# Kernel optimization log

Measured on AMD Instinct MI355X. Metric: run time of the kernel, lower is better.

Reference implementation:

```python
import jax, jax.numpy as jnp
import numpy as np
from jax import lax


def _conv(x, w, b, padding):
    # x: NCHW, w: OIHW
    y = lax.conv_general_dilated(x, w, (1, 1), padding,
                                 dimension_numbers=('NCHW', 'OIHW', 'NCHW'))
    return y + b[None, :, None, None]


def setup_inputs() -> dict:
    key = jax.random.key(0)
    ks = jax.random.split(key, 24)
    B = 64
    d = {
        'p2': jax.random.normal(ks[0], (B, 128, 64, 128), jnp.float32),
        'p3': jax.random.normal(ks[1], (B, 128, 32, 64), jnp.float32),
        'p4': jax.random.normal(ks[2], (B, 128, 16, 32), jnp.float32),
        'p5': jax.random.normal(ks[3], (B, 512, 8, 16), jnp.float32),
    }
    def w(k, shape, fan_in):
        return jax.random.normal(k, shape, jnp.float32) * (1.0 / np.sqrt(fan_in))
    # smooth convs 3x3, 128->128
    for i, name in enumerate(['s1', 's2', 's3']):
        d['w_' + name] = w(ks[4 + 2 * i], (128, 128, 3, 3), 128 * 9)
        d['b_' + name] = jnp.zeros((128,), jnp.float32)
    # tidy convs 1x1
    tidy_cin = [128, 128, 128, 512]
    for i in range(4):
        d['w_t%d' % (i + 1)] = w(ks[10 + i], (1, tidy_cin[i], 1, 1), tidy_cin[i])
        d['b_t%d' % (i + 1)] = jnp.zeros((1,), jnp.float32)
    # pl convs (kH,1) on single channel
    pl_kh = [64, 32, 16, 8]
    for i in range(4):
        d['w_pl%d' % (i + 1)] = w(ks[14 + i], (1, 1, pl_kh[i], 1), pl_kh[i])
        d['b_pl%d' % (i + 1)] = jnp.zeros((1,), jnp.float32)
    return d


def reference(p2, p3, p4, p5,
              w_s1, b_s1, w_s2, b_s2, w_s3, b_s3,
              w_t1, b_t1, w_t2, b_t2, w_t3, b_t3, w_t4, b_t4,
              w_pl1, b_pl1, w_pl2, b_pl2, w_pl3, b_pl3, w_pl4, b_pl4):
    B = p2.shape[0]
    # smooth + relu (p5 has no smooth in the original module)
    q2 = jax.nn.relu(_conv(p2, w_s1, b_s1, 'SAME'))
    q3 = jax.nn.relu(_conv(p3, w_s2, b_s2, 'SAME'))
    q4 = jax.nn.relu(_conv(p4, w_s3, b_s3, 'SAME'))
    # tidy 1x1 -> single score channel
    t1 = _conv(q2, w_t1, b_t1, 'VALID')
    t2 = _conv(q3, w_t2, b_t2, 'VALID')
    t3 = _conv(q4, w_t3, b_t3, 'VALID')
    t4 = _conv(p5, w_t4, b_t4, 'VALID')
    # column-pooling convs collapse height to 1 -> per-column scores
    c1 = _conv(t1, w_pl1, b_pl1, 'VALID').reshape(B, -1)  # [B,128]
    c2 = _conv(t2, w_pl2, b_pl2, 'VALID').reshape(B, -1)  # [B,64]
    c3 = _conv(t3, w_pl3, b_pl3, 'VALID').reshape(B, -1)  # [B,32]
    c4 = _conv(t4, w_pl4, b_pl4, 'VALID').reshape(B, -1)  # [B,16]
    return jnp.concatenate([c1, c2, c3, c4], axis=1)      # [B,240]
```

## Files before the change

### kernel.cpp

```cpp
#include <hip/hip_runtime.h>


typedef short s8v __attribute__((ext_vector_type(8)));
typedef float f4v __attribute__((ext_vector_type(4)));

#define BARRIER() asm volatile("s_waitcnt lgkmcnt(0)\n\ts_barrier" ::: "memory")

__device__ __forceinline__ unsigned short f32_bf16_rne(float f) {
  union { float f; unsigned int u; } v;
  v.f = f;
  unsigned int u = v.u;
  u += 0x7FFFu + ((u >> 16) & 1u);
  return (unsigned short)(u >> 16);
}

__global__ void prep_w_k(const float* __restrict__ w1,
                         const float* __restrict__ w2,
                         const float* __restrict__ w3,
                         unsigned short* __restrict__ out) {
  int idx = blockIdx.x * 256 + threadIdx.x;
  if (idx >= 442368) return;
  int i    = idx & 7;
  int cout = (idx >> 3) & 127;
  int t    = idx >> 10;
  int qg = t & 3; t >>= 2;
  int kw = t % 3; t /= 3;
  int kh = t % 3; t /= 3;
  int chunk = t & 3; t >>= 2;
  int s = t;
  const float* w = (s == 0) ? w1 : ((s == 1) ? w2 : w3);
  int cin = chunk * 32 + qg * 8 + i;
  out[idx] = f32_bf16_rne(w[((cout * 128 + cin) * 3 + kh) * 3 + kw]);
}

__global__ void init_out_k(float* __restrict__ out,
                           const float* bt1, const float* bt2,
                           const float* bt3, const float* bt4,
                           const float* wpl1, const float* bpl1,
                           const float* wpl2, const float* bpl2,
                           const float* wpl3, const float* bpl3,
                           const float* wpl4, const float* bpl4) {
  int idx = blockIdx.x * 256 + threadIdx.x;
  if (idx >= 64 * 240) return;
  int c = idx % 240;
  const float* wpl; const float* bpl; const float* bt; int H;
  if (c < 128)      { wpl = wpl1; bpl = bpl1; bt = bt1; H = 64; }
  else if (c < 192) { wpl = wpl2; bpl = bpl2; bt = bt2; H = 32; }
  else if (c < 224) { wpl = wpl3; bpl = bpl3; bt = bt3; H = 16; }
  else              { wpl = wpl4; bpl = bpl4; bt = bt4; H = 8;  }
  float s = 0.f;
  for (int h = 0; h < H; ++h) s += wpl[h];
  out[idx] = bt[0] * s + bpl[0];
}

__global__ void level4_k(const float* __restrict__ p5,
                         const float* __restrict__ w_t4,
                         const float* __restrict__ w_pl4,
                         float* __restrict__ out) {
  int b = blockIdx.x;
  int z = blockIdx.y;
  int t = threadIdx.x;
  int w = t & 15, g = t >> 4;
  const float* base = p5 + (size_t)b * 65536 + z * 16384;
  const float* wt = w_t4 + z * 128;
  float acc = 0.f;
  for (int j = g; j < 1024; j += 16) {
    acc += wt[j >> 3] * w_pl4[j & 7] * base[j * 16 + w];
  }
  acc += __shfl_xor(acc, 16);
  acc += __shfl_xor(acc, 32);
  if ((t & 48) == 0) atomicAdd(&out[b * 240 + 224 + w], acc);
}

template<int H, int W, int COLBASE>
__global__ __launch_bounds__(512, 1)
void conv_fused_k(const float* __restrict__ p,
                  const unsigned short* __restrict__ wl,
                  const float* __restrict__ b_s,
                  const float* __restrict__ w_t,
                  const float* __restrict__ w_pl,
                  float* __restrict__ out) {
  constexpr int R  = 4;
  constexpr int WP = W + 2;
  constexpr int HW = H * W;
  constexpr int WN = W / 16;
  constexpr int WM = 8 / WN;
  constexpr int MT = 8 / WM;
  constexpr int SLOTS = 2 * 4 * W;
  constexpr int SPT = (SLOTS + 511) / 512;

  __shared__ __align__(16) unsigned short Xs[2][4][6][WP][8];
  __shared__ __align__(16) unsigned short Ws[2][3][4][128][8];

  const int tid  = threadIdx.x;
  const int wave = tid >> 6, lane = tid & 63;
  const int lm = lane & 15, q = lane >> 4;
  const int mw = wave / WN, ns = wave % WN;
  const int hb = blockIdx.x * R;
  const int b  = blockIdx.y;
  const float* pb = p + (size_t)b * 128 * HW;

  bool sok[SPT];
  int  h0k[SPT];
  int  xbase[SPT];
  const float* sbase[SPT];
#pragma unroll
  for (int k = 0; k < SPT; ++k) {
    int slot = tid + 512 * k;
    sok[k] = (SLOTS % 512 == 0) ? true : (slot < SLOTS);
    int rk = slot / (4 * W);
    int qg = (slot / W) & 3;
    int wp = slot % W;
    h0k[k]   = hb - 1 + rk;
    xbase[k] = ((qg * 6 + rk) * WP + 1 + wp) * 8;
    sbase[k] = pb + (size_t)(qg * 8) * HW + wp;
  }

  float xf[SPT][8];
  s8v wreg[3];
  const unsigned short* wseg = wl + tid * 24;
  unsigned short* wdst = &Ws[0][0][0][0][0] + tid * 24;

  auto issueW = [&](int t) {
    const unsigned short* s = wseg + t * 12288;
#pragma unroll
    for (int j = 0; j < 3; ++j) wreg[j] = *(const s8v*)(s + j * 8);
  };
  auto writeW = [&](int buf) {
    unsigned short* d = wdst + buf * 12288;
#pragma unroll
    for (int j = 0; j < 3; ++j) *(s8v*)(d + j * 8) = wreg[j];
  };
  auto issueXa = [&](float (*arr)[8], int chunk, int kh) {
#pragma unroll
    for (int k = 0; k < SPT; ++k) {
      int hin = h0k[k] + 2 * kh;
      bool ok = sok[k] && ((unsigned)hin < (unsigned)H);
      if (ok) {
        const float* s = sbase[k] + (size_t)chunk * (32 * HW) + (size_t)hin * W;
#pragma unroll
        for (int i = 0; i < 8; ++i) arr[k][i] = s[(size_t)i * HW];
      } else {
#pragma unroll
        for (int i = 0; i < 8; ++i) arr[k][i] = 0.f;
      }
    }
  };
  auto writeXa = [&](float (*arr)[8], int buf, int kh) {
    unsigned short* dst = &Xs[buf][0][0][0][0] + 2 * kh * (WP * 8);
#pragma unroll
    for (int k = 0; k < SPT; ++k) {
      if (sok[k]) {
        s8v v;
#pragma unroll
        for (int i = 0; i < 8; ++i) v[i] = (short)f32_bf16_rne(arr[k][i]);
        *(s8v*)(dst + xbase[k]) = v;
      }
    }
  };

  if (tid < 96) {
    int t = tid;
    int pos = (t & 1) ? (WP - 1) : 0; t >>= 1;
    int sl = t % 6; t /= 6;
    int qg = t & 3; int bf = t >> 2;
    const s8v Z = {0, 0, 0, 0, 0, 0, 0, 0};
    *(s8v*)&Xs[bf][qg][sl][pos][0] = Z;
  }
  {
    float x0[SPT][8], x1[SPT][8], x2[SPT][8];
    issueW(0);
    issueXa(x0, 0, 0);
    issueXa(x1, 0, 1);
    issueXa(x2, 0, 2);
    writeW(0);
    issueW(1);
    writeXa(x0, 0, 0);
    writeXa(x1, 0, 1);
    writeXa(x2, 0, 2);
    issueXa(xf, 1, 0);
  }
  BARRIER();

  f4v acc[R][MT];
#pragma unroll
  for (int r = 0; r < R; ++r)
#pragma unroll
    for (int mt = 0; mt < MT; ++mt)
      acc[r][mt] = (f4v){0.f, 0.f, 0.f, 0.f};

  const int ncol = ns * 16 + lm;

  for (int c = 0; c < 4; ++c) {
#pragma unroll
    for (int kh = 0; kh < 3; ++kh) {
      const int sidx = c * 3 + kh;
      if (sidx < 11) writeW((sidx + 1) & 1);
      if (sidx < 10) issueW(sidx + 2);
      if (c < 3) writeXa(xf, (c + 1) & 1, kh);
      if (kh < 2) { if (c < 3) issueXa(xf, c + 1, kh + 1); }
      else        { if (c < 2) issueXa(xf, c + 2, 0); }

      const unsigned short* WsRd = &Ws[sidx & 1][0][0][0][0];
      const unsigned short* XsRd = &Xs[c & 1][0][0][0][0];
      __builtin_amdgcn_s_setprio(1);
#pragma unroll
      for (int kw = 0; kw < 3; ++kw) {
        s8v af[MT];
#pragma unroll
        for (int mt = 0; mt < MT; ++mt)
          af[mt] = *(const s8v*)(WsRd + kw * 4096 + q * 1024 +
                                 ((mw * MT + mt) * 16 + lm) * 8);
#pragma unroll
        for (int r = 0; r < R; ++r) {
          const s8v bfv = *(const s8v*)(XsRd + ((q * 6 + (kh + r)) * WP + (ncol + kw)) * 8);
#pragma unroll
          for (int mt = 0; mt < MT; ++mt)
            acc[r][mt] = __builtin_amdgcn_mfma_f32_16x16x32_bf16(af[mt], bfv, acc[r][mt], 0, 0, 0);
        }
      }
      __builtin_amdgcn_s_setprio(0);
      if (sidx < 11) BARRIER();
    }
  }

  float stot = 0.f;
#pragma unroll
  for (int r = 0; r < R; ++r) {
    float s = 0.f;
#pragma unroll
    for (int mt = 0; mt < MT; ++mt) {
#pragma unroll
      for (int rg = 0; rg < 4; ++rg) {
        int cout = (mw * MT + mt) * 16 + q * 4 + rg;
        float v = fmaxf(acc[r][mt][rg] + b_s[cout], 0.f);
        s = fmaf(w_t[cout], v, s);
      }
    }
    stot = fmaf(w_pl[hb + r], s, stot);
  }
  stot += __shfl_xor(stot, 16);
  stot += __shfl_xor(stot, 32);
  if (lane < 16) atomicAdd(&out[b * 240 + COLBASE + ncol], stot);
}

extern "C" void kernel_launch(void* const* d_in, const int* in_sizes, int n_in,
                              void* d_out, int out_size, void* d_ws, size_t ws_size,
                              hipStream_t stream) {
  (void)in_sizes; (void)n_in; (void)out_size; (void)ws_size;
  const float* p2   = (const float*)d_in[0];
  const float* p3   = (const float*)d_in[1];
  const float* p4   = (const float*)d_in[2];
  const float* p5   = (const float*)d_in[3];
  const float* w_s1 = (const float*)d_in[4];
  const float* b_s1 = (const float*)d_in[5];
  const float* w_s2 = (const float*)d_in[6];
  const float* b_s2 = (const float*)d_in[7];
  const float* w_s3 = (const float*)d_in[8];
  const float* b_s3 = (const float*)d_in[9];
  const float* w_t1 = (const float*)d_in[10];
  const float* b_t1 = (const float*)d_in[11];
  const float* w_t2 = (const float*)d_in[12];
  const float* b_t2 = (const float*)d_in[13];
  const float* w_t3 = (const float*)d_in[14];
  const float* b_t3 = (const float*)d_in[15];
  const float* w_t4 = (const float*)d_in[16];
  const float* b_t4 = (const float*)d_in[17];
  const float* w_pl1 = (const float*)d_in[18];
  const float* b_pl1 = (const float*)d_in[19];
  const float* w_pl2 = (const float*)d_in[20];
  const float* b_pl2 = (const float*)d_in[21];
  const float* w_pl3 = (const float*)d_in[22];
  const float* b_pl3 = (const float*)d_in[23];
  const float* w_pl4 = (const float*)d_in[24];
  const float* b_pl4 = (const float*)d_in[25];

  unsigned short* wp = (unsigned short*)d_ws;
  float* out = (float*)d_out;

  prep_w_k<<<dim3(1728), dim3(256), 0, stream>>>(w_s1, w_s2, w_s3, wp);
  init_out_k<<<dim3(60), dim3(256), 0, stream>>>(out, b_t1, b_t2, b_t3, b_t4,
                                                 w_pl1, b_pl1, w_pl2, b_pl2,
                                                 w_pl3, b_pl3, w_pl4, b_pl4);
  conv_fused_k<64, 128, 0><<<dim3(16, 64), dim3(512), 0, stream>>>(
      p2, wp, b_s1, w_t1, w_pl1, out);
  conv_fused_k<32, 64, 128><<<dim3(8, 64), dim3(512), 0, stream>>>(
      p3, wp + 147456, b_s2, w_t2, w_pl2, out);
  conv_fused_k<16, 32, 192><<<dim3(4, 64), dim3(512), 0, stream>>>(
      p4, wp + 294912, b_s3, w_t3, w_pl3, out);
  level4_k<<<dim3(64, 4), dim3(256), 0, stream>>>(p5, w_t4, w_pl4, out);
}
```

Baseline: 727.4 us.

## Shrink conv blocks to 256 threads with per-level row tiles and multi-column waves

The fused 3x3 conv kernels now run with 256 threads (4 waves) per block instead of 512. The largest level switches to 2 output rows per block, which doubles the grid. Each wave now covers several 16-column N tiles, so each B fragment is reused across more accumulators. The staging buffer, halo zeroing, weight-copy pattern and epilogue are generalised to the variable row count. The aim is better occupancy and load balance with smaller per-block LDS, traded against more halo re-reads for level 1 and more per-thread load work.

```diff
diff --git a/kernel.cpp b/kernel.cpp
--- a/kernel.cpp
+++ b/kernel.cpp
@@ -73,23 +73,25 @@
 }
 
 template<int H, int W, int COLBASE>
-__global__ __launch_bounds__(512, 1)
+__global__ __launch_bounds__(256, 1)
 void conv_fused_k(const float* __restrict__ p,
                   const unsigned short* __restrict__ wl,
                   const float* __restrict__ b_s,
                   const float* __restrict__ w_t,
                   const float* __restrict__ w_pl,
                   float* __restrict__ out) {
-  constexpr int R  = 4;
+  constexpr int R  = (W == 128) ? 2 : 4;
+  constexpr int RS = R + 2;
+  constexpr int NB = RS / 2;
   constexpr int WP = W + 2;
   constexpr int HW = H * W;
-  constexpr int WN = W / 16;
-  constexpr int WM = 8 / WN;
+  constexpr int WN = (W >= 64) ? 4 : 2;
+  constexpr int WM = 4 / WN;
+  constexpr int NT = (W / 16) / WN;
   constexpr int MT = 8 / WM;
-  constexpr int SLOTS = 2 * 4 * W;
-  constexpr int SPT = (SLOTS + 511) / 512;
-
-  __shared__ __align__(16) unsigned short Xs[2][4][6][WP][8];
+  constexpr int SPT = (2 * 4 * W) / 256;
+
+  __shared__ __align__(16) unsigned short Xs[2][4][RS][WP][8];
   __shared__ __align__(16) unsigned short Ws[2][3][4][128][8];
 
   const int tid  = threadIdx.x;
@@ -100,43 +102,38 @@
   const int b  = blockIdx.y;
   const float* pb = p + (size_t)b * 128 * HW;
 
-  bool sok[SPT];
-  int  h0k[SPT];
-  int  xbase[SPT];
-  const float* sbase[SPT];
+  int rk0[SPT]; int xb[SPT]; const float* sbase[SPT];
 #pragma unroll
   for (int k = 0; k < SPT; ++k) {
-    int slot = tid + 512 * k;
-    sok[k] = (SLOTS % 512 == 0) ? true : (slot < SLOTS);
+    int slot = tid + 256 * k;
     int rk = slot / (4 * W);
     int qg = (slot / W) & 3;
     int wp = slot % W;
-    h0k[k]   = hb - 1 + rk;
-    xbase[k] = ((qg * 6 + rk) * WP + 1 + wp) * 8;
+    rk0[k] = rk;
+    xb[k]  = ((qg * RS + rk) * WP + 1 + wp) * 8;
     sbase[k] = pb + (size_t)(qg * 8) * HW + wp;
   }
 
   float xf[SPT][8];
-  s8v wreg[3];
-  const unsigned short* wseg = wl + tid * 24;
-  unsigned short* wdst = &Ws[0][0][0][0][0] + tid * 24;
+  s8v wreg[6];
+  const unsigned short* wseg = wl + wave * 512 + lane * 8;
+  unsigned short* wdst = &Ws[0][0][0][0][0] + wave * 512 + lane * 8;
 
   auto issueW = [&](int t) {
     const unsigned short* s = wseg + t * 12288;
 #pragma unroll
-    for (int j = 0; j < 3; ++j) wreg[j] = *(const s8v*)(s + j * 8);
+    for (int j = 0; j < 6; ++j) wreg[j] = *(const s8v*)(s + j * 2048);
   };
   auto writeW = [&](int buf) {
     unsigned short* d = wdst + buf * 12288;
 #pragma unroll
-    for (int j = 0; j < 3; ++j) *(s8v*)(d + j * 8) = wreg[j];
-  };
-  auto issueXa = [&](float (*arr)[8], int chunk, int kh) {
+    for (int j = 0; j < 6; ++j) *(s8v*)(d + j * 2048) = wreg[j];
+  };
+  auto issueXa = [&](float (*arr)[8], int chunk, int burst) {
 #pragma unroll
     for (int k = 0; k < SPT; ++k) {
-      int hin = h0k[k] + 2 * kh;
-      bool ok = sok[k] && ((unsigned)hin < (unsigned)H);
-      if (ok) {
+      int hin = hb - 1 + 2 * burst + rk0[k];
+      if ((unsigned)hin < (unsigned)H) {
         const float* s = sbase[k] + (size_t)chunk * (32 * HW) + (size_t)hin * W;
 #pragma unroll
         for (int i = 0; i < 8; ++i) arr[k][i] = s[(size_t)i * HW];
@@ -146,50 +143,47 @@
       }
     }
   };
-  auto writeXa = [&](float (*arr)[8], int buf, int kh) {
-    unsigned short* dst = &Xs[buf][0][0][0][0] + 2 * kh * (WP * 8);
+  auto writeXa = [&](float (*arr)[8], int buf, int burst) {
+    unsigned short* dst = &Xs[buf][0][0][0][0] + 2 * burst * (WP * 8);
 #pragma unroll
     for (int k = 0; k < SPT; ++k) {
-      if (sok[k]) {
-        s8v v;
-#pragma unroll
-        for (int i = 0; i < 8; ++i) v[i] = (short)f32_bf16_rne(arr[k][i]);
-        *(s8v*)(dst + xbase[k]) = v;
-      }
-    }
-  };
-
-  if (tid < 96) {
-    int t = tid;
-    int pos = (t & 1) ? (WP - 1) : 0; t >>= 1;
-    int sl = t % 6; t /= 6;
-    int qg = t & 3; int bf = t >> 2;
+      s8v v;
+#pragma unroll
+      for (int i = 0; i < 8; ++i) v[i] = (short)f32_bf16_rne(arr[k][i]);
+      *(s8v*)(dst + xb[k]) = v;
+    }
+  };
+
+  if (tid < 16 * RS) {
+    int idx = tid;
+    int bf  = idx / (8 * RS); int rem = idx % (8 * RS);
+    int qg  = rem / (2 * RS); int r2  = rem % (2 * RS);
+    int sl  = r2 >> 1;
+    int pos = (r2 & 1) ? (WP - 1) : 0;
     const s8v Z = {0, 0, 0, 0, 0, 0, 0, 0};
     *(s8v*)&Xs[bf][qg][sl][pos][0] = Z;
   }
   {
-    float x0[SPT][8], x1[SPT][8], x2[SPT][8];
+    float xp[NB][SPT][8];
     issueW(0);
-    issueXa(x0, 0, 0);
-    issueXa(x1, 0, 1);
-    issueXa(x2, 0, 2);
+#pragma unroll
+    for (int j = 0; j < NB; ++j) issueXa(xp[j], 0, j);
     writeW(0);
     issueW(1);
-    writeXa(x0, 0, 0);
-    writeXa(x1, 0, 1);
-    writeXa(x2, 0, 2);
+#pragma unroll
+    for (int j = 0; j < NB; ++j) writeXa(xp[j], 0, j);
     issueXa(xf, 1, 0);
   }
   BARRIER();
 
-  f4v acc[R][MT];
+  f4v acc[R][MT][NT];
 #pragma unroll
   for (int r = 0; r < R; ++r)
 #pragma unroll
     for (int mt = 0; mt < MT; ++mt)
-      acc[r][mt] = (f4v){0.f, 0.f, 0.f, 0.f};
-
-  const int ncol = ns * 16 + lm;
+#pragma unroll
+      for (int t = 0; t < NT; ++t)
+        acc[r][mt][t] = (f4v){0.f, 0.f, 0.f, 0.f};
 
   for (int c = 0; c < 4; ++c) {
 #pragma unroll
@@ -197,9 +191,9 @@
       const int sidx = c * 3 + kh;
       if (sidx < 11) writeW((sidx + 1) & 1);
       if (sidx < 10) issueW(sidx + 2);
-      if (c < 3) writeXa(xf, (c + 1) & 1, kh);
-      if (kh < 2) { if (c < 3) issueXa(xf, c + 1, kh + 1); }
-      else        { if (c < 2) issueXa(xf, c + 2, 0); }
+      if (kh < NB) { if (c < 3) writeXa(xf, (c + 1) & 1, kh); }
+      if (kh + 1 < NB) { if (c < 3) issueXa(xf, c + 1, kh + 1); }
+      else if (kh == 2) { if (c < 2) issueXa(xf, c + 2, 0); }
 
       const unsigned short* WsRd = &Ws[sidx & 1][0][0][0][0];
       const unsigned short* XsRd = &Xs[c & 1][0][0][0][0];
@@ -212,36 +206,42 @@
           af[mt] = *(const s8v*)(WsRd + kw * 4096 + q * 1024 +
                                  ((mw * MT + mt) * 16 + lm) * 8);
 #pragma unroll
-        for (int r = 0; r < R; ++r) {
-          const s8v bfv = *(const s8v*)(XsRd + ((q * 6 + (kh + r)) * WP + (ncol + kw)) * 8);
-#pragma unroll
-          for (int mt = 0; mt < MT; ++mt)
-            acc[r][mt] = __builtin_amdgcn_mfma_f32_16x16x32_bf16(af[mt], bfv, acc[r][mt], 0, 0, 0);
-        }
+        for (int r = 0; r < R; ++r)
+#pragma unroll
+          for (int t = 0; t < NT; ++t) {
+            const int n = (ns * NT + t) * 16 + lm;
+            const s8v bfv = *(const s8v*)(XsRd + ((q * RS + (kh + r)) * WP + (n + kw)) * 8);
+#pragma unroll
+            for (int mt = 0; mt < MT; ++mt)
+              acc[r][mt][t] = __builtin_amdgcn_mfma_f32_16x16x32_bf16(af[mt], bfv, acc[r][mt][t], 0, 0, 0);
+          }
       }
       __builtin_amdgcn_s_setprio(0);
       if (sidx < 11) BARRIER();
     }
   }
 
-  float stot = 0.f;
-#pragma unroll
-  for (int r = 0; r < R; ++r) {
-    float s = 0.f;
-#pragma unroll
-    for (int mt = 0; mt < MT; ++mt) {
-#pragma unroll
-      for (int rg = 0; rg < 4; ++rg) {
-        int cout = (mw * MT + mt) * 16 + q * 4 + rg;
-        float v = fmaxf(acc[r][mt][rg] + b_s[cout], 0.f);
-        s = fmaf(w_t[cout], v, s);
+#pragma unroll
+  for (int t = 0; t < NT; ++t) {
+    float stot = 0.f;
+#pragma unroll
+    for (int r = 0; r < R; ++r) {
+      float s = 0.f;
+#pragma unroll
+      for (int mt = 0; mt < MT; ++mt) {
+#pragma unroll
+        for (int rg = 0; rg < 4; ++rg) {
+          int cout = (mw * MT + mt) * 16 + q * 4 + rg;
+          float v = fmaxf(acc[r][mt][t][rg] + b_s[cout], 0.f);
+          s = fmaf(w_t[cout], v, s);
+        }
       }
-    }
-    stot = fmaf(w_pl[hb + r], s, stot);
-  }
-  stot += __shfl_xor(stot, 16);
-  stot += __shfl_xor(stot, 32);
-  if (lane < 16) atomicAdd(&out[b * 240 + COLBASE + ncol], stot);
+      stot = fmaf(w_pl[hb + r], s, stot);
+    }
+    stot += __shfl_xor(stot, 16);
+    stot += __shfl_xor(stot, 32);
+    if (lane < 16) atomicAdd(&out[b * 240 + COLBASE + (ns * NT + t) * 16 + lm], stot);
+  }
 }
 
 extern "C" void kernel_launch(void* const* d_in, const int* in_sizes, int n_in,
@@ -282,11 +282,11 @@
   init_out_k<<<dim3(60), dim3(256), 0, stream>>>(out, b_t1, b_t2, b_t3, b_t4,
                                                  w_pl1, b_pl1, w_pl2, b_pl2,
                                                  w_pl3, b_pl3, w_pl4, b_pl4);
-  conv_fused_k<64, 128, 0><<<dim3(16, 64), dim3(512), 0, stream>>>(
+  conv_fused_k<64, 128, 0><<<dim3(32, 64), dim3(256), 0, stream>>>(
       p2, wp, b_s1, w_t1, w_pl1, out);
-  conv_fused_k<32, 64, 128><<<dim3(8, 64), dim3(512), 0, stream>>>(
+  conv_fused_k<32, 64, 128><<<dim3(8, 64), dim3(256), 0, stream>>>(
       p3, wp + 147456, b_s2, w_t2, w_pl2, out);
-  conv_fused_k<16, 32, 192><<<dim3(4, 64), dim3(512), 0, stream>>>(
+  conv_fused_k<16, 32, 192><<<dim3(4, 64), dim3(256), 0, stream>>>(
       p4, wp + 294912, b_s3, w_t3, w_pl3, out);
   level4_k<<<dim3(64, 4), dim3(256), 0, stream>>>(p5, w_t4, w_pl4, out);
 }
```

Result: faster. 646.6 us (-11.1%).
